# Performance work log

Measured on AMD Instinct MI355X. Metric: run time of the kernel, lower is better.

## Reference

```python
import math
import jax, jax.numpy as jnp
import numpy as np

B, S, H, BOT, RD, N, K = 4, 2048, 1024, 128, 48, 4096, 8

def setup_inputs() -> dict:
    key = jax.random.key(0)
    ks = jax.random.split(key, 12)
    hidden_states = jax.random.normal(ks[0], (B, S, H), jnp.float32)
    q_proj_w = jax.random.normal(ks[1], (BOT, H), jnp.float32) * (1.0 / math.sqrt(H))
    router_w = jax.random.normal(ks[2], (RD, BOT), jnp.float32) * (1.0 / math.sqrt(BOT))
    aux_keys = jax.random.normal(ks[3], (N, BOT), jnp.float32) * 0.01
    aux_values = jax.random.normal(ks[4], (N, H), jnp.float32) * 0.02
    # reliability per slot (log-domain additive mask derived from lifecycle state)
    reliability_mask = jax.random.uniform(ks[5], (N,), jnp.float32)
    unc_w1 = jax.random.normal(ks[6], (H // 4, H), jnp.float32) * (1.0 / math.sqrt(H))
    unc_b1 = jnp.zeros((H // 4,), jnp.float32)
    unc_w2 = jax.random.normal(ks[7], (1, H // 4), jnp.float32) * 0.02
    unc_b2 = jnp.zeros((1,), jnp.float32)
    gate_w1 = jnp.asarray(0.5, jnp.float32)
    gate_bias = jnp.asarray(-1.0, jnp.float32)
    return {"hidden_states": hidden_states, "q_proj_w": q_proj_w, "router_w": router_w,
            "aux_keys": aux_keys, "aux_values": aux_values, "reliability_mask": reliability_mask,
            "unc_w1": unc_w1, "unc_b1": unc_b1, "unc_w2": unc_w2, "unc_b2": unc_b2,
            "gate_w1": gate_w1, "gate_bias": gate_bias}

def reference(hidden_states, q_proj_w, router_w, aux_keys, aux_values, reliability_mask,
              unc_w1, unc_b1, unc_w2, unc_b2, gate_w1, gate_bias):
    # --- SlotRouter: project query/keys to router_dim, score, mask, top-k ---
    query = jnp.einsum('bsh,dh->bsd', hidden_states, q_proj_w)        # [B,S,BOT]
    rq = jnp.einsum('bsd,rd->bsr', query, router_w)                   # [B,S,RD]
    rk = jnp.einsum('nd,rd->nr', aux_keys, router_w)                  # [N,RD]
    scores = jnp.einsum('bsr,nr->bsn', rq, rk) / math.sqrt(RD)        # [B,S,N]
    scores = scores + reliability_mask[None, None, :]
    top_scores, top_idx = jax.lax.top_k(scores, K)                    # [B,S,K]
    # --- UncertaintyEstimator (HIDDEN_VARIANCE) ---
    mean = hidden_states.mean(axis=-1, keepdims=True)
    variance = ((hidden_states - mean) ** 2).mean(axis=-1)            # [B,S]
    log_var = jnp.log1p(variance)
    normalized_var = log_var / (log_var.mean() + 1e-6)
    h1 = jax.nn.gelu(jnp.einsum('bsh,fh->bsf', hidden_states, unc_w1) + unc_b1, approximate=False)
    learned = (jnp.einsum('bsf,of->bso', h1, unc_w2) + unc_b2)[..., 0]
    uncertainty = jnp.clip(normalized_var * 0.5 + jax.nn.sigmoid(learned) * 2.5, 0.0, 5.0)
    # --- Gate-1 scalar gate + slot aggregation ---
    gate = jax.nn.sigmoid(gate_w1 * uncertainty + gate_bias)          # [B,S]
    w = jax.nn.softmax(top_scores, axis=-1)                           # [B,S,K]
    v = aux_values[top_idx]                                           # [B,S,K,H]
    agg = jnp.einsum('bsk,bskh->bsh', w, v)
    out = hidden_states + gate[..., None] * agg
    return out
```

## Files before the change

### kernel.cpp

```cpp
#include <hip/hip_runtime.h>
#include <hip/hip_bf16.h>
#include <math.h>
#include <stdint.h>

#define NT 256
constexpr int Hc = 1024, BOTc = 128, RDc = 48, Nc = 4096;
constexpr int ROWS = 8192;
constexpr float INV_SQRT_RD = 0.14433756729740643f;

typedef short bf16x8 __attribute__((ext_vector_type(8)));
typedef float f32x4 __attribute__((ext_vector_type(4)));

__device__ __forceinline__ uint32_t umin32(uint32_t a, uint32_t b) { return a < b ? a : b; }
__device__ __forceinline__ uint32_t umax32(uint32_t a, uint32_t b) { return a > b ? a : b; }
__device__ __forceinline__ void ce_asc(uint32_t& x, uint32_t& y) {
  uint32_t lo = umin32(x, y), hi = umax32(x, y); x = lo; y = hi;
}
__device__ __forceinline__ uint32_t pack_score(float s, int slot) {
  uint32_t u = __float_as_uint(s);
  u = (u & 0x80000000u) ? ~u : (u | 0x80000000u);
  return (u & 0xFFFFF000u) | (uint32_t)slot;
}
__device__ __forceinline__ float unpack_score(uint32_t p) {
  uint32_t m = p & 0xFFFFF000u;
  uint32_t f = (m & 0x80000000u) ? (m ^ 0x80000000u) : ~m;
  return __uint_as_float(f);
}
__device__ __forceinline__ void merge_top8(uint32_t a[8], const uint32_t b[8]) {
  uint32_t m[8];
#pragma unroll
  for (int i = 0; i < 8; ++i) m[i] = umax32(a[i], b[7 - i]);
  ce_asc(m[0], m[4]); ce_asc(m[1], m[5]); ce_asc(m[2], m[6]); ce_asc(m[3], m[7]);
  ce_asc(m[0], m[2]); ce_asc(m[1], m[3]); ce_asc(m[4], m[6]); ce_asc(m[5], m[7]);
  ce_asc(m[0], m[1]); ce_asc(m[2], m[3]); ce_asc(m[4], m[5]); ce_asc(m[6], m[7]);
#pragma unroll
  for (int i = 0; i < 8; ++i) a[i] = m[i];
}
__device__ __forceinline__ void top8_insert(uint32_t top[8], uint32_t p) {
  if (p > top[0]) {
    top[0] = p;
    ce_asc(top[0], top[1]); ce_asc(top[1], top[2]); ce_asc(top[2], top[3]);
    ce_asc(top[3], top[4]); ce_asc(top[4], top[5]); ce_asc(top[5], top[6]);
    ce_asc(top[6], top[7]);
  }
}
__device__ __forceinline__ uint16_t bf16bits(float x) {
  uint32_t u = __float_as_uint(x);
  return (uint16_t)(((u + 0x7FFFu + ((u >> 16) & 1u)) >> 16) & 0xFFFFu);
}
__device__ __forceinline__ float bf2f(uint16_t h) {
  return __uint_as_float((uint32_t)h << 16);
}

constexpr int GP_HB = 2048, GP_CVT = 544, GP_W48 = 64, GP_RK = 768;
__global__ __launch_bounds__(256) void k_prep_all(
    const float* __restrict__ hidden, const float* __restrict__ q_proj_w,
    const float* __restrict__ router_w, const float* __restrict__ aux_keys,
    const float* __restrict__ aux_values, const float* __restrict__ rel,
    const float* __restrict__ unc_w1,
    uint16_t* __restrict__ xb, float* __restrict__ log_var,
    uint16_t* __restrict__ wcat, uint16_t* __restrict__ avb,
    uint16_t* __restrict__ rk_b) {
  int bid = blockIdx.x;
  int tid = threadIdx.x;
  if (bid < GP_HB) {
    int wave = tid >> 6, lane = tid & 63;
    int row = bid * 4 + wave;
    const float4* hrow = reinterpret_cast<const float4*>(hidden + (size_t)row * Hc);
    float4 v[4];
#pragma unroll
    for (int i = 0; i < 4; ++i) v[i] = hrow[lane + 64 * i];
    float s = 0.f, q = 0.f;
#pragma unroll
    for (int i = 0; i < 4; ++i) {
      ushort4 h;
      h.x = bf16bits(v[i].x); h.y = bf16bits(v[i].y);
      h.z = bf16bits(v[i].z); h.w = bf16bits(v[i].w);
      *reinterpret_cast<ushort4*>(xb + (size_t)row * Hc + (lane + 64 * i) * 4) = h;
      s += v[i].x + v[i].y + v[i].z + v[i].w;
      q += v[i].x * v[i].x + v[i].y * v[i].y + v[i].z * v[i].z + v[i].w * v[i].w;
    }
#pragma unroll
    for (int d = 32; d >= 1; d >>= 1) { s += __shfl_down(s, d); q += __shfl_down(q, d); }
    if (lane == 0) {
      float mean = s * (1.f / Hc);
      float var = q * (1.f / Hc) - mean * mean;
      log_var[row] = log1pf(var);
    }
    return;
  }
  bid -= GP_HB;
  if (bid < GP_CVT) {
    const int W1Q = 256 * Hc / 4;
#pragma unroll
    for (int i = 0; i < 8; ++i) {
      int idx = bid * 2048 + i * 256 + tid;
      float4 v; ushort4 h;
      if (idx < W1Q) {
        v = reinterpret_cast<const float4*>(unc_w1)[idx];
        h.x = bf16bits(v.x); h.y = bf16bits(v.y); h.z = bf16bits(v.z); h.w = bf16bits(v.w);
        reinterpret_cast<ushort4*>(wcat)[idx] = h;
      } else {
        int j = idx - W1Q;
        v = reinterpret_cast<const float4*>(aux_values)[j];
        h.x = bf16bits(v.x); h.y = bf16bits(v.y); h.z = bf16bits(v.z); h.w = bf16bits(v.w);
        reinterpret_cast<ushort4*>(avb)[j] = h;
      }
    }
    return;
  }
  bid -= GP_CVT;
  if (bid < GP_W48) {
    __shared__ float rw[BOTc];
    int j = bid;
    if (j >= RDc) {
      for (int hh = tid; hh < Hc; hh += NT) wcat[(size_t)(256 + j) * Hc + hh] = 0;
      return;
    }
    for (int d = tid; d < BOTc; d += NT) rw[d] = router_w[j * BOTc + d];
    __syncthreads();
    for (int hh = tid; hh < Hc; hh += NT) {
      float acc = 0.f;
#pragma unroll 8
      for (int d = 0; d < BOTc; ++d) acc = fmaf(rw[d], q_proj_w[d * Hc + hh], acc);
      wcat[(size_t)(256 + j) * Hc + hh] = bf16bits(acc);
    }
    return;
  }
  bid -= GP_W48;
  {
    int gid = bid * NT + tid;
    int n = gid / RDc, r = gid - n * RDc;
    float acc = 0.f;
#pragma unroll 8
    for (int d = 0; d < BOTc; ++d)
      acc = fmaf(aux_keys[n * BOTc + d], router_w[r * BOTc + d], acc);
    rk_b[(size_t)n * 64 + r] = bf16bits(acc * INV_SQRT_RD);
    if (r < 16) rk_b[(size_t)n * 64 + 48 + r] = (r == 0) ? bf16bits(rel[n]) : (uint16_t)0;
  }
}

__global__ __launch_bounds__(256) void k_xw(const uint16_t* __restrict__ xb,
                                            const uint16_t* __restrict__ wcat,
                                            const float* __restrict__ b1,
                                            const float* __restrict__ w2,
                                            float* __restrict__ uncp,
                                            uint16_t* __restrict__ rq_b) {
  __shared__ uint16_t As[2][64 * 72];
  __shared__ uint16_t Bs[2][64 * 72];
  int bid = blockIdx.x;
  int wid = (bid & 7) * 80 + (bid >> 3);
  int rowg = wid / 5, colg = wid - rowg * 5;
  int tid = threadIdx.x, wave = tid >> 6, lane = tid & 63;
  int l15 = lane & 15, lg = lane >> 4;
  int wr = wave >> 1, wc = wave & 1;
  int row0 = rowg * 64, n0 = colg * 64;
  int srow = tid >> 3, sseg = tid & 7;
  const uint16_t* agp = xb + (size_t)(row0 + srow) * Hc + sseg * 8;
  const uint16_t* bgp = wcat + (size_t)(n0 + srow) * Hc + sseg * 8;
  int sboff = srow * 72 + sseg * 8;
  int arow = wr * 32 + l15, brow = wc * 32 + l15;

  bf16x8 ra0 = *reinterpret_cast<const bf16x8*>(agp);
  bf16x8 ra1 = *reinterpret_cast<const bf16x8*>(agp + (size_t)32 * Hc);
  bf16x8 rb0 = *reinterpret_cast<const bf16x8*>(bgp);
  bf16x8 rb1 = *reinterpret_cast<const bf16x8*>(bgp + (size_t)32 * Hc);
  f32x4 acc00 = {0.f,0.f,0.f,0.f}, acc01 = {0.f,0.f,0.f,0.f};
  f32x4 acc10 = {0.f,0.f,0.f,0.f}, acc11 = {0.f,0.f,0.f,0.f};

  for (int t = 0; t < 16; ++t) {
    int buf = t & 1;
    *reinterpret_cast<bf16x8*>(&As[buf][sboff]) = ra0;
    *reinterpret_cast<bf16x8*>(&As[buf][sboff + 32 * 72]) = ra1;
    *reinterpret_cast<bf16x8*>(&Bs[buf][sboff]) = rb0;
    *reinterpret_cast<bf16x8*>(&Bs[buf][sboff + 32 * 72]) = rb1;
    if (t < 15) {
      int k0 = (t + 1) * 64;
      ra0 = *reinterpret_cast<const bf16x8*>(agp + k0);
      ra1 = *reinterpret_cast<const bf16x8*>(agp + (size_t)32 * Hc + k0);
      rb0 = *reinterpret_cast<const bf16x8*>(bgp + k0);
      rb1 = *reinterpret_cast<const bf16x8*>(bgp + (size_t)32 * Hc + k0);
    }
    __syncthreads();
#pragma unroll
    for (int ks = 0; ks < 2; ++ks) {
      bf16x8 a0 = *reinterpret_cast<const bf16x8*>(&As[buf][arow * 72 + ks * 32 + lg * 8]);
      bf16x8 a1 = *reinterpret_cast<const bf16x8*>(&As[buf][(arow + 16) * 72 + ks * 32 + lg * 8]);
      bf16x8 b0 = *reinterpret_cast<const bf16x8*>(&Bs[buf][brow * 72 + ks * 32 + lg * 8]);
      bf16x8 b1f = *reinterpret_cast<const bf16x8*>(&Bs[buf][(brow + 16) * 72 + ks * 32 + lg * 8]);
      acc00 = __builtin_amdgcn_mfma_f32_16x16x32_bf16(a0, b0, acc00, 0, 0, 0);
      acc01 = __builtin_amdgcn_mfma_f32_16x16x32_bf16(a0, b1f, acc01, 0, 0, 0);
      acc10 = __builtin_amdgcn_mfma_f32_16x16x32_bf16(a1, b0, acc10, 0, 0, 0);
      acc11 = __builtin_amdgcn_mfma_f32_16x16x32_bf16(a1, b1f, acc11, 0, 0, 0);
    }
    __syncthreads();
  }
  if (colg < 4) {
    int gc0 = n0 + wc * 32 + l15;
    float b1v0 = b1[gc0],      w2v0 = w2[gc0];
    float b1v1 = b1[gc0 + 16], w2v1 = w2[gc0 + 16];
    int strip = colg * 2 + wc;
    float part0[4], part1[4];
#pragma unroll
    for (int r = 0; r < 4; ++r) {
      float x00 = acc00[r] + b1v0, x01 = acc01[r] + b1v1;
      float x10 = acc10[r] + b1v0, x11 = acc11[r] + b1v1;
      float g00 = 0.5f * x00 * (1.f + erff(x00 * 0.70710678118654752f));
      float g01 = 0.5f * x01 * (1.f + erff(x01 * 0.70710678118654752f));
      float g10 = 0.5f * x10 * (1.f + erff(x10 * 0.70710678118654752f));
      float g11 = 0.5f * x11 * (1.f + erff(x11 * 0.70710678118654752f));
      part0[r] = fmaf(g00, w2v0, g01 * w2v1);
      part1[r] = fmaf(g10, w2v0, g11 * w2v1);
    }
#pragma unroll
    for (int d = 1; d < 16; d <<= 1)
#pragma unroll
      for (int r = 0; r < 4; ++r) {
        part0[r] += __shfl_xor(part0[r], d);
        part1[r] += __shfl_xor(part1[r], d);
      }
    if (l15 == 0) {
#pragma unroll
      for (int r = 0; r < 4; ++r) {
        uncp[(size_t)(row0 + wr * 32 + lg * 4 + r) * 8 + strip] = part0[r];
        uncp[(size_t)(row0 + wr * 32 + 16 + lg * 4 + r) * 8 + strip] = part1[r];
      }
    }
  } else {
    int colA = wc * 32 + l15, colB = colA + 16;
#pragma unroll
    for (int r = 0; r < 4; ++r) {
      int rA = row0 + wr * 32 + lg * 4 + r, rB = rA + 16;
      uint16_t vA = bf16bits(acc00[r]);
      uint16_t vB = (colB == 48) ? (uint16_t)0x3F80u : bf16bits(acc01[r]);
      uint16_t uA = bf16bits(acc10[r]);
      uint16_t uB = (colB == 48) ? (uint16_t)0x3F80u : bf16bits(acc11[r]);
      rq_b[(size_t)rA * 64 + colA] = vA;
      rq_b[(size_t)rA * 64 + colB] = vB;
      rq_b[(size_t)rB * 64 + colA] = uA;
      rq_b[(size_t)rB * 64 + colB] = uB;
    }
  }
}

__global__ __launch_bounds__(256) void k_scores_mfma(const uint16_t* __restrict__ rq_b,
                                                     const uint16_t* __restrict__ rk_b,
                                                     uint32_t* __restrict__ cand,
                                                     const float* __restrict__ log_var,
                                                     float* __restrict__ stats) {
  int tid = threadIdx.x;
  if (blockIdx.x == 1024) {
    float s = 0.f;
    for (int i = tid; i < ROWS; i += NT) s += log_var[i];
#pragma unroll
    for (int d = 32; d >= 1; d >>= 1) s += __shfl_down(s, d);
    __shared__ float ls[4];
    int lane = tid & 63, wid = tid >> 6;
    if (lane == 0) ls[wid] = s;
    __syncthreads();
    if (tid == 0) {
      s = ls[0] + ls[1] + ls[2] + ls[3];
      stats[0] = 1.f / (s * (1.f / ROWS) + 1e-6f);
    }
    return;
  }
  int wave = tid >> 6, lane = tid & 63;
  int l15 = lane & 15, lg = lane >> 4;
  int rowg = blockIdx.x >> 3, range = blockIdx.x & 7;
  int q0 = rowg * 64 + wave * 16;
  const uint16_t* qp = rq_b + (size_t)(q0 + l15) * 64 + lg * 8;
  bf16x8 qf1 = *reinterpret_cast<const bf16x8*>(qp);
  bf16x8 qf2 = *reinterpret_cast<const bf16x8*>(qp + 32);
  uint32_t top[8];
#pragma unroll
  for (int q = 0; q < 8; ++q) top[q] = 0u;
  int sbase = range * 512;
  const uint16_t* kp = rk_b + (size_t)(sbase + l15) * 64 + lg * 8;
  bf16x8 a1c = *reinterpret_cast<const bf16x8*>(kp);
  bf16x8 a2c = *reinterpret_cast<const bf16x8*>(kp + 32);
  bf16x8 a3c = *reinterpret_cast<const bf16x8*>(kp + 1024);
  bf16x8 a4c = *reinterpret_cast<const bf16x8*>(kp + 1024 + 32);
#pragma unroll
  for (int t = 0; t < 32; t += 2) {
    bf16x8 a1n, a2n, a3n, a4n;
    if (t < 30) {
      const uint16_t* kpn = kp + (size_t)(t + 2) * 1024;
      a1n = *reinterpret_cast<const bf16x8*>(kpn);
      a2n = *reinterpret_cast<const bf16x8*>(kpn + 32);
      a3n = *reinterpret_cast<const bf16x8*>(kpn + 1024);
      a4n = *reinterpret_cast<const bf16x8*>(kpn + 1024 + 32);
    }
    int s0 = sbase + t * 16;
    f32x4 acc0 = {0.f,0.f,0.f,0.f}, acc1 = {0.f,0.f,0.f,0.f};
    acc0 = __builtin_amdgcn_mfma_f32_16x16x32_bf16(a1c, qf1, acc0, 0, 0, 0);
    acc1 = __builtin_amdgcn_mfma_f32_16x16x32_bf16(a3c, qf1, acc1, 0, 0, 0);
    acc0 = __builtin_amdgcn_mfma_f32_16x16x32_bf16(a2c, qf2, acc0, 0, 0, 0);
    acc1 = __builtin_amdgcn_mfma_f32_16x16x32_bf16(a4c, qf2, acc1, 0, 0, 0);
#pragma unroll
    for (int r = 0; r < 4; ++r) top8_insert(top, pack_score(acc0[r], s0 + lg * 4 + r));
#pragma unroll
    for (int r = 0; r < 4; ++r) top8_insert(top, pack_score(acc1[r], s0 + 16 + lg * 4 + r));
    if (t < 30) { a1c = a1n; a2c = a2n; a3c = a3n; a4c = a4n; }
  }
#pragma unroll
  for (int dd = 16; dd <= 32; dd <<= 1) {
    uint32_t o[8];
#pragma unroll
    for (int q = 0; q < 8; ++q) o[q] = __shfl_xor(top[q], dd);
    merge_top8(top, o);
  }
  if (lg == 0) {
    int row = q0 + l15;
#pragma unroll
    for (int q = 0; q < 8; ++q) cand[((size_t)row * 8 + range) * 8 + q] = top[q];
  }
}

__global__ __launch_bounds__(256) void k_final(const float* __restrict__ hidden,
                                               const uint16_t* __restrict__ avb,
                                               const uint32_t* __restrict__ cand,
                                               const float* __restrict__ log_var,
                                               const float* __restrict__ uncp,
                                               const float* __restrict__ stats,
                                               const float* __restrict__ b2,
                                               const float* __restrict__ gw,
                                               const float* __restrict__ gb,
                                               float* __restrict__ out) {
  int row = blockIdx.x;
  int tid = threadIdx.x;
  __shared__ float ws_[8]; __shared__ int wi_[8]; __shared__ float sgate;
  if (tid < 64) {
    int lane = tid;
    uint32_t l[8];
    float up = 0.f;
    if (lane < 8) {
      const uint32_t* c = cand + (size_t)row * 64 + lane * 8;
#pragma unroll
      for (int q = 0; q < 8; ++q) l[q] = c[q];
      up = uncp[(size_t)row * 8 + lane];
    } else {
#pragma unroll
      for (int q = 0; q < 8; ++q) l[q] = 0u;
    }
#pragma unroll
    for (int d = 1; d < 8; d <<= 1) {
      uint32_t o[8];
#pragma unroll
      for (int q = 0; q < 8; ++q) o[q] = __shfl_xor(l[q], d);
      merge_top8(l, o);
      up += __shfl_xor(up, d);
    }
    if (lane == 0) {
      float sc[8];
#pragma unroll
      for (int q = 0; q < 8; ++q) sc[q] = unpack_score(l[q]);
      float mx = sc[7];
      float e[8]; float sum = 0.f;
#pragma unroll
      for (int q = 0; q < 8; ++q) { e[q] = expf(sc[q] - mx); sum += e[q]; }
      float inv = 1.f / sum;
#pragma unroll
      for (int q = 0; q < 8; ++q) { ws_[q] = e[q] * inv; wi_[q] = (int)(l[q] & 0xFFFu); }
      float learned = up + b2[0];
      float nv = log_var[row] * stats[0];
      float sig = 1.f / (1.f + expf(-learned));
      float u = nv * 0.5f + sig * 2.5f;
      u = fminf(fmaxf(u, 0.f), 5.f);
      sgate = 1.f / (1.f + expf(-(gw[0] * u + gb[0])));
    }
  }
  __syncthreads();
  int h0 = tid * 4;
  float4 hv = *reinterpret_cast<const float4*>(hidden + (size_t)row * Hc + h0);
  float ax = 0.f, ay = 0.f, az = 0.f, aw = 0.f;
#pragma unroll
  for (int k = 0; k < 8; ++k) {
    float w = ws_[k];
    ushort4 v = *reinterpret_cast<const ushort4*>(avb + (size_t)wi_[k] * Hc + h0);
    ax = fmaf(w, bf2f(v.x), ax); ay = fmaf(w, bf2f(v.y), ay);
    az = fmaf(w, bf2f(v.z), az); aw = fmaf(w, bf2f(v.w), aw);
  }
  float g = sgate;
  float4 o;
  o.x = hv.x + g * ax; o.y = hv.y + g * ay; o.z = hv.z + g * az; o.w = hv.w + g * aw;
  *reinterpret_cast<float4*>(out + (size_t)row * Hc + h0) = o;
}

extern "C" void kernel_launch(void* const* d_in, const int* in_sizes, int n_in,
                              void* d_out, int out_size, void* d_ws, size_t ws_size,
                              hipStream_t stream) {
  const float* hidden     = (const float*)d_in[0];
  const float* q_proj_w   = (const float*)d_in[1];
  const float* router_w   = (const float*)d_in[2];
  const float* aux_keys   = (const float*)d_in[3];
  const float* aux_values = (const float*)d_in[4];
  const float* rel        = (const float*)d_in[5];
  const float* unc_w1     = (const float*)d_in[6];
  const float* unc_b1     = (const float*)d_in[7];
  const float* unc_w2     = (const float*)d_in[8];
  const float* unc_b2     = (const float*)d_in[9];
  const float* gate_w1    = (const float*)d_in[10];
  const float* gate_bias  = (const float*)d_in[11];
  float* out = (float*)d_out;

  uint8_t* w = (uint8_t*)d_ws;
  uint16_t* xb    = (uint16_t*)w;                 w += (size_t)ROWS * Hc * 2;
  uint16_t* wcat  = (uint16_t*)w;                 w += (size_t)320 * Hc * 2;
  uint16_t* avb   = (uint16_t*)w;                 w += (size_t)Nc * Hc * 2;
  uint16_t* rq_b  = (uint16_t*)w;                 w += (size_t)ROWS * 64 * 2;
  uint16_t* rk_b  = (uint16_t*)w;                 w += (size_t)Nc * 64 * 2;
  float* log_var  = (float*)w;                    w += (size_t)ROWS * 4;
  float* uncp     = (float*)w;                    w += (size_t)ROWS * 8 * 4;
  float* stats    = (float*)w;                    w += 256;
  uint32_t* cand  = (uint32_t*)w;                 w += (size_t)ROWS * 64 * 4;

  k_prep_all<<<GP_HB + GP_CVT + GP_W48 + GP_RK, NT, 0, stream>>>(
      hidden, q_proj_w, router_w, aux_keys, aux_values, rel, unc_w1,
      xb, log_var, wcat, avb, rk_b);
  k_xw<<<640, NT, 0, stream>>>(xb, wcat, unc_b1, unc_w2, uncp, rq_b);
  k_scores_mfma<<<1025, NT, 0, stream>>>(rq_b, rk_b, cand, log_var, stats);
  k_final<<<ROWS, NT, 0, stream>>>(hidden, avb, cand, log_var, uncp,
                                   stats, unc_b2, gate_w1, gate_bias, out);
}
```

Before: 114.0 us.

## Reorder prep blocks, batch loads, and read bf16 residual in final kernel

```diff
diff --git a/kernel.cpp b/kernel.cpp
--- a/kernel.cpp
+++ b/kernel.cpp
@@ -52,7 +52,7 @@
   return __uint_as_float((uint32_t)h << 16);
 }
 
-constexpr int GP_HB = 2048, GP_CVT = 544, GP_W48 = 64, GP_RK = 768;
+constexpr int GP_W48 = 64, GP_RK = 768, GP_HB = 1024, GP_CVW = 32, GP_CVA = 512;
 __global__ __launch_bounds__(256) void k_prep_all(
     const float* __restrict__ hidden, const float* __restrict__ q_proj_w,
     const float* __restrict__ router_w, const float* __restrict__ aux_keys,
@@ -63,53 +63,6 @@
     uint16_t* __restrict__ rk_b) {
   int bid = blockIdx.x;
   int tid = threadIdx.x;
-  if (bid < GP_HB) {
-    int wave = tid >> 6, lane = tid & 63;
-    int row = bid * 4 + wave;
-    const float4* hrow = reinterpret_cast<const float4*>(hidden + (size_t)row * Hc);
-    float4 v[4];
-#pragma unroll
-    for (int i = 0; i < 4; ++i) v[i] = hrow[lane + 64 * i];
-    float s = 0.f, q = 0.f;
-#pragma unroll
-    for (int i = 0; i < 4; ++i) {
-      ushort4 h;
-      h.x = bf16bits(v[i].x); h.y = bf16bits(v[i].y);
-      h.z = bf16bits(v[i].z); h.w = bf16bits(v[i].w);
-      *reinterpret_cast<ushort4*>(xb + (size_t)row * Hc + (lane + 64 * i) * 4) = h;
-      s += v[i].x + v[i].y + v[i].z + v[i].w;
-      q += v[i].x * v[i].x + v[i].y * v[i].y + v[i].z * v[i].z + v[i].w * v[i].w;
-    }
-#pragma unroll
-    for (int d = 32; d >= 1; d >>= 1) { s += __shfl_down(s, d); q += __shfl_down(q, d); }
-    if (lane == 0) {
-      float mean = s * (1.f / Hc);
-      float var = q * (1.f / Hc) - mean * mean;
-      log_var[row] = log1pf(var);
-    }
-    return;
-  }
-  bid -= GP_HB;
-  if (bid < GP_CVT) {
-    const int W1Q = 256 * Hc / 4;
-#pragma unroll
-    for (int i = 0; i < 8; ++i) {
-      int idx = bid * 2048 + i * 256 + tid;
-      float4 v; ushort4 h;
-      if (idx < W1Q) {
-        v = reinterpret_cast<const float4*>(unc_w1)[idx];
-        h.x = bf16bits(v.x); h.y = bf16bits(v.y); h.z = bf16bits(v.z); h.w = bf16bits(v.w);
-        reinterpret_cast<ushort4*>(wcat)[idx] = h;
-      } else {
-        int j = idx - W1Q;
-        v = reinterpret_cast<const float4*>(aux_values)[j];
-        h.x = bf16bits(v.x); h.y = bf16bits(v.y); h.z = bf16bits(v.z); h.w = bf16bits(v.w);
-        reinterpret_cast<ushort4*>(avb)[j] = h;
-      }
-    }
-    return;
-  }
-  bid -= GP_CVT;
   if (bid < GP_W48) {
     __shared__ float rw[BOTc];
     int j = bid;
@@ -119,16 +72,21 @@
     }
     for (int d = tid; d < BOTc; d += NT) rw[d] = router_w[j * BOTc + d];
     __syncthreads();
-    for (int hh = tid; hh < Hc; hh += NT) {
-      float acc = 0.f;
-#pragma unroll 8
-      for (int d = 0; d < BOTc; ++d) acc = fmaf(rw[d], q_proj_w[d * Hc + hh], acc);
-      wcat[(size_t)(256 + j) * Hc + hh] = bf16bits(acc);
-    }
+    float acc[4] = {0.f, 0.f, 0.f, 0.f};
+#pragma unroll 4
+    for (int d = 0; d < BOTc; ++d) {
+      float r = rw[d];
+#pragma unroll
+      for (int jj = 0; jj < 4; ++jj)
+        acc[jj] = fmaf(r, q_proj_w[d * Hc + tid + 256 * jj], acc[jj]);
+    }
+#pragma unroll
+    for (int jj = 0; jj < 4; ++jj)
+      wcat[(size_t)(256 + j) * Hc + tid + 256 * jj] = bf16bits(acc[jj]);
     return;
   }
   bid -= GP_W48;
-  {
+  if (bid < GP_RK) {
     int gid = bid * NT + tid;
     int n = gid / RDc, r = gid - n * RDc;
     float acc = 0.f;
@@ -137,6 +95,78 @@
       acc = fmaf(aux_keys[n * BOTc + d], router_w[r * BOTc + d], acc);
     rk_b[(size_t)n * 64 + r] = bf16bits(acc * INV_SQRT_RD);
     if (r < 16) rk_b[(size_t)n * 64 + 48 + r] = (r == 0) ? bf16bits(rel[n]) : (uint16_t)0;
+    return;
+  }
+  bid -= GP_RK;
+  if (bid < GP_HB) {
+    int wave = tid >> 6, lane = tid & 63;
+    int row = bid * 8 + wave * 2;
+    const float4* r0 = reinterpret_cast<const float4*>(hidden + (size_t)row * Hc);
+    const float4* r1 = reinterpret_cast<const float4*>(hidden + (size_t)(row + 1) * Hc);
+    float4 v0[4], v1[4];
+#pragma unroll
+    for (int i = 0; i < 4; ++i) v0[i] = r0[lane + 64 * i];
+#pragma unroll
+    for (int i = 0; i < 4; ++i) v1[i] = r1[lane + 64 * i];
+    float s0 = 0.f, q0 = 0.f, s1 = 0.f, q1 = 0.f;
+#pragma unroll
+    for (int i = 0; i < 4; ++i) {
+      ushort4 h;
+      h.x = bf16bits(v0[i].x); h.y = bf16bits(v0[i].y);
+      h.z = bf16bits(v0[i].z); h.w = bf16bits(v0[i].w);
+      *reinterpret_cast<ushort4*>(xb + (size_t)row * Hc + (lane + 64 * i) * 4) = h;
+      s0 += v0[i].x + v0[i].y + v0[i].z + v0[i].w;
+      q0 += v0[i].x * v0[i].x + v0[i].y * v0[i].y + v0[i].z * v0[i].z + v0[i].w * v0[i].w;
+    }
+#pragma unroll
+    for (int i = 0; i < 4; ++i) {
+      ushort4 h;
+      h.x = bf16bits(v1[i].x); h.y = bf16bits(v1[i].y);
+      h.z = bf16bits(v1[i].z); h.w = bf16bits(v1[i].w);
+      *reinterpret_cast<ushort4*>(xb + (size_t)(row + 1) * Hc + (lane + 64 * i) * 4) = h;
+      s1 += v1[i].x + v1[i].y + v1[i].z + v1[i].w;
+      q1 += v1[i].x * v1[i].x + v1[i].y * v1[i].y + v1[i].z * v1[i].z + v1[i].w * v1[i].w;
+    }
+#pragma unroll
+    for (int d = 32; d >= 1; d >>= 1) {
+      s0 += __shfl_down(s0, d); q0 += __shfl_down(q0, d);
+      s1 += __shfl_down(s1, d); q1 += __shfl_down(q1, d);
+    }
+    if (lane == 0) {
+      float m0 = s0 * (1.f / Hc), m1 = s1 * (1.f / Hc);
+      log_var[row]     = log1pf(q0 * (1.f / Hc) - m0 * m0);
+      log_var[row + 1] = log1pf(q1 * (1.f / Hc) - m1 * m1);
+    }
+    return;
+  }
+  bid -= GP_HB;
+  if (bid < GP_CVW) {
+    float4 v[8];
+    int base = bid * 2048 + tid;
+#pragma unroll
+    for (int i = 0; i < 8; ++i) v[i] = reinterpret_cast<const float4*>(unc_w1)[base + i * 256];
+#pragma unroll
+    for (int i = 0; i < 8; ++i) {
+      ushort4 h;
+      h.x = bf16bits(v[i].x); h.y = bf16bits(v[i].y);
+      h.z = bf16bits(v[i].z); h.w = bf16bits(v[i].w);
+      reinterpret_cast<ushort4*>(wcat)[base + i * 256] = h;
+    }
+    return;
+  }
+  bid -= GP_CVW;
+  {
+    float4 v[8];
+    int base = bid * 2048 + tid;
+#pragma unroll
+    for (int i = 0; i < 8; ++i) v[i] = reinterpret_cast<const float4*>(aux_values)[base + i * 256];
+#pragma unroll
+    for (int i = 0; i < 8; ++i) {
+      ushort4 h;
+      h.x = bf16bits(v[i].x); h.y = bf16bits(v[i].y);
+      h.z = bf16bits(v[i].z); h.w = bf16bits(v[i].w);
+      reinterpret_cast<ushort4*>(avb)[base + i * 256] = h;
+    }
   }
 }
 
@@ -316,7 +346,7 @@
   }
 }
 
-__global__ __launch_bounds__(256) void k_final(const float* __restrict__ hidden,
+__global__ __launch_bounds__(256) void k_final(const uint16_t* __restrict__ xb,
                                                const uint16_t* __restrict__ avb,
                                                const uint32_t* __restrict__ cand,
                                                const float* __restrict__ log_var,
@@ -371,7 +401,7 @@
   }
   __syncthreads();
   int h0 = tid * 4;
-  float4 hv = *reinterpret_cast<const float4*>(hidden + (size_t)row * Hc + h0);
+  ushort4 hb = *reinterpret_cast<const ushort4*>(xb + (size_t)row * Hc + h0);
   float ax = 0.f, ay = 0.f, az = 0.f, aw = 0.f;
 #pragma unroll
   for (int k = 0; k < 8; ++k) {
@@ -382,7 +412,8 @@
   }
   float g = sgate;
   float4 o;
-  o.x = hv.x + g * ax; o.y = hv.y + g * ay; o.z = hv.z + g * az; o.w = hv.w + g * aw;
+  o.x = bf2f(hb.x) + g * ax; o.y = bf2f(hb.y) + g * ay;
+  o.z = bf2f(hb.z) + g * az; o.w = bf2f(hb.w) + g * aw;
   *reinterpret_cast<float4*>(out + (size_t)row * Hc + h0) = o;
 }
 
@@ -414,11 +445,11 @@
   float* stats    = (float*)w;                    w += 256;
   uint32_t* cand  = (uint32_t*)w;                 w += (size_t)ROWS * 64 * 4;
 
-  k_prep_all<<<GP_HB + GP_CVT + GP_W48 + GP_RK, NT, 0, stream>>>(
+  k_prep_all<<<GP_W48 + GP_RK + GP_HB + GP_CVW + GP_CVA, NT, 0, stream>>>(
       hidden, q_proj_w, router_w, aux_keys, aux_values, rel, unc_w1,
       xb, log_var, wcat, avb, rk_b);
   k_xw<<<640, NT, 0, stream>>>(xb, wcat, unc_b1, unc_w2, uncp, rq_b);
   k_scores_mfma<<<1025, NT, 0, stream>>>(rq_b, rk_b, cand, log_var, stats);
-  k_final<<<ROWS, NT, 0, stream>>>(hidden, avb, cand, log_var, uncp,
+  k_final<<<ROWS, NT, 0, stream>>>(xb, avb, cand, log_var, uncp,
                                    stats, unc_b2, gate_w1, gate_bias, out);
 }
```

New measurement: 98.61 us. 1.16x faster.
